# Kernel optimization log

Measured on AMD Instinct MI355X. Metric: run time of the kernel, lower is better.

Reference implementation:

```python
import jax, jax.numpy as jnp
import numpy as np

N = 100000          # nodes
E = 1000000         # edges (before self loops)
F_IN = 128          # node feature dim
HEADS = [4, 2, 2]   # gat_heads
D = 48              # per-head out channels (hardcoded in module)
G = 64              # number of graphs in batch
FC_DIM = 192
OUT_DIM = 96
NEG_SLOPE = 0.2     # PyG GATConv default


def setup_inputs() -> dict:
    key = jax.random.key(0)
    ks = jax.random.split(key, 32)
    d = {
        "x": jax.random.normal(ks[0], (N, F_IN), jnp.float32),
        "edge_index": jax.random.randint(ks[1], (2, E), 0, N, dtype=jnp.int64),
        "batch": jnp.sort(jax.random.randint(ks[2], (N,), 0, G, dtype=jnp.int64)),
    }
    in_ch = F_IN
    k = 3
    for i, h in enumerate(HEADS):
        d[f"W{i}"] = jax.random.normal(ks[k], (in_ch, h * D), jnp.float32) / np.sqrt(in_ch); k += 1
        d[f"att_src{i}"] = jax.random.normal(ks[k], (h, D), jnp.float32) * 0.1; k += 1
        d[f"att_dst{i}"] = jax.random.normal(ks[k], (h, D), jnp.float32) * 0.1; k += 1
        d[f"bias{i}"] = jnp.zeros((h * D,), jnp.float32)
        in_ch = h * D
    d["fcW1"] = jax.random.normal(ks[k], (in_ch, FC_DIM), jnp.float32) / np.sqrt(in_ch); k += 1
    d["fcb1"] = jnp.zeros((FC_DIM,), jnp.float32)
    d["fcW2"] = jax.random.normal(ks[k], (FC_DIM, OUT_DIM), jnp.float32) / np.sqrt(FC_DIM); k += 1
    d["fcb2"] = jnp.zeros((OUT_DIM,), jnp.float32)
    return d


def _gat_layer(x, W, att_src, att_dst, bias, src, dst, heads):
    n = x.shape[0]
    h = (x @ W).reshape(n, heads, D)                    # [N,H,D]
    a_src = jnp.sum(h * att_src, axis=-1)               # [N,H]
    a_dst = jnp.sum(h * att_dst, axis=-1)               # [N,H]
    e = jax.nn.leaky_relu(a_src[src] + a_dst[dst], NEG_SLOPE)   # [Et,H]
    # segment softmax over incoming edges at each destination node
    m = jax.ops.segment_max(e, dst, num_segments=n)
    e = jnp.exp(e - m[dst])
    denom = jax.ops.segment_sum(e, dst, num_segments=n)
    alpha = e / (denom[dst] + 1e-16)                    # [Et,H]
    msg = h[src] * alpha[..., None]                     # [Et,H,D]
    out = jax.ops.segment_sum(msg, dst, num_segments=n) # [N,H,D]
    return out.reshape(n, heads * D) + bias


def reference(x, edge_index, batch,
              W0, att_src0, att_dst0, bias0,
              W1, att_src1, att_dst1, bias1,
              W2, att_src2, att_dst2, bias2,
              fcW1, fcb1, fcW2, fcb2):
    n = x.shape[0]
    loops = jnp.arange(n, dtype=edge_index.dtype)
    src = jnp.concatenate([edge_index[0], loops])   # add self loops (PyG default)
    dst = jnp.concatenate([edge_index[1], loops])
    x = jax.nn.relu(_gat_layer(x, W0, att_src0, att_dst0, bias0, src, dst, HEADS[0]))
    x = jax.nn.relu(_gat_layer(x, W1, att_src1, att_dst1, bias1, src, dst, HEADS[1]))
    x = jax.nn.relu(_gat_layer(x, W2, att_src2, att_dst2, bias2, src, dst, HEADS[2]))
    # global mean pool over graphs
    sums = jax.ops.segment_sum(x, batch, num_segments=G)
    counts = jax.ops.segment_sum(jnp.ones((n, 1), x.dtype), batch, num_segments=G)
    pooled = sums / jnp.maximum(counts, 1.0)
    h = jax.nn.relu(pooled @ fcW1 + fcb1)
    return h @ fcW2 + fcb2
```

## Files before the change

### kernel.cpp

```cpp
#include <hip/hip_runtime.h>

#define CAP 48
#define DD 48
#define BSH 8
#define NBUCK_MAX 400
#define CHUNK_MAX 4300

typedef short v8s __attribute__((ext_vector_type(8)));
typedef float v4f __attribute__((ext_vector_type(4)));
typedef float v2f __attribute__((ext_vector_type(2)));

__device__ __forceinline__ unsigned int bf16r(float f) {
    unsigned int u = __float_as_uint(f);
    return (u + 0x7FFFu + ((u >> 16) & 1u)) >> 16;
}

__device__ __forceinline__ v8s ld_frag(const ushort* p) {
    const uint2* q = reinterpret_cast<const uint2*>(p);
    uint2 a = q[0], b = q[1];
    union { unsigned int u[4]; v8s v; } t;
    t.u[0] = a.x; t.u[1] = a.y; t.u[2] = b.x; t.u[3] = b.y;
    return t.v;
}


__global__ void hist_kernel(const int* __restrict__ ei, int E, int N, int nbuck,
                            int* __restrict__ Hh) {
    __shared__ int lhist[NBUCK_MAX];
    int blk = blockIdx.x, t = threadIdx.x;
    int Et = E + N;
    int chunk = (Et + 255) >> 8;
    int lo = blk * chunk, hi = min(Et, lo + chunk);
    for (int i = t; i < nbuck; i += 256) lhist[i] = 0;
    __syncthreads();
    for (int e = lo + t; e < hi; e += 256) {
        int d = (e < E) ? ei[E + e] : (e - E);
        atomicAdd(&lhist[d >> BSH], 1);
    }
    __syncthreads();
    for (int b = t; b < nbuck; b += 256) Hh[b * 256 + blk] = lhist[b];
}

__global__ void scan_bucket_kernel(int* __restrict__ Hh, int* __restrict__ btot) {
    int b = blockIdx.x, lane = threadIdx.x;
    uint4 v = reinterpret_cast<uint4*>(Hh)[b * 64 + lane];
    unsigned s0 = v.x, s1 = s0 + v.y, s2 = s1 + v.z, s3 = s2 + v.w;
    unsigned incl = s3;
#pragma unroll
    for (int off = 1; off < 64; off <<= 1) {
        unsigned tmp = __shfl_up(incl, off);
        if (lane >= off) incl += tmp;
    }
    unsigned excl = incl - s3;
    reinterpret_cast<uint4*>(Hh)[b * 64 + lane] =
        make_uint4(excl, excl + s0, excl + s1, excl + s2);
    if (lane == 63) btot[b] = (int)incl;
}

__global__ void scan_base_kernel(const int* __restrict__ btot, int* __restrict__ bbase, int nbuck) {
    int lane = threadIdx.x;
    int carry = 0;
    int nch = (nbuck + 63) >> 6;
    for (int c = 0; c < nch; c++) {
        int idx = c * 64 + lane;
        int val = (idx < nbuck) ? btot[idx] : 0;
        int incl = val;
#pragma unroll
        for (int off = 1; off < 64; off <<= 1) {
            int tmp = __shfl_up(incl, off);
            if (lane >= off) incl += tmp;
        }
        if (idx < nbuck) bbase[idx] = carry + incl - val;
        carry += __shfl(incl, 63);
    }
    if (lane == 0) bbase[nbuck] = carry;
}

__global__ void add_base_kernel(int* __restrict__ Hh, const int* __restrict__ bbase) {
    Hh[blockIdx.x * 256 + threadIdx.x] += bbase[blockIdx.x];
}

__global__ void scatter_kernel(const int* __restrict__ ei, int E, int N, int nbuck,
                               const int* __restrict__ Hh, unsigned int* __restrict__ P) {
    __shared__ unsigned int sp[CHUNK_MAX];
    __shared__ int ga[CHUNK_MAX];
    __shared__ int lhist[NBUCK_MAX], lbaseL[NBUCK_MAX], lbaseG[NBUCK_MAX], lcur[NBUCK_MAX];
    int blk = blockIdx.x, t = threadIdx.x;
    int Et = E + N;
    int chunk = (Et + 255) >> 8;
    int lo = blk * chunk, hi = min(Et, lo + chunk);
    for (int i = t; i < nbuck; i += 256) { lhist[i] = 0; lcur[i] = 0; }
    __syncthreads();
    for (int e = lo + t; e < hi; e += 256) {
        int d = (e < E) ? ei[E + e] : (e - E);
        atomicAdd(&lhist[d >> BSH], 1);
    }
    __syncthreads();
    if (t < 64) {
        int lane = t, carry = 0;
        int nch = (nbuck + 63) >> 6;
        for (int c = 0; c < nch; c++) {
            int idx = c * 64 + lane;
            int val = (idx < nbuck) ? lhist[idx] : 0;
            int incl = val;
#pragma unroll
            for (int off = 1; off < 64; off <<= 1) {
                int tmp = __shfl_up(incl, off);
                if (lane >= off) incl += tmp;
            }
            if (idx < nbuck) {
                lbaseL[idx] = carry + incl - val;
                lbaseG[idx] = Hh[idx * 256 + blk];
            }
            carry += __shfl(incl, 63);
        }
    }
    __syncthreads();
    for (int e = lo + t; e < hi; e += 256) {
        int s, d;
        if (e < E) { s = ei[e]; d = ei[E + e]; } else { s = e - E; d = e - E; }
        int b = d >> BSH;
        int lpos = atomicAdd(&lcur[b], 1);
        int loc = lbaseL[b] + lpos;
        sp[loc] = ((unsigned)(d & 255) << 24) | (unsigned)s;
        ga[loc] = lbaseG[b] + lpos;
    }
    __syncthreads();
    int len = hi - lo;
    for (int i = t; i < len; i += 256) P[ga[i]] = sp[i];
}

__global__ void buildadj_kernel(const unsigned int* __restrict__ P, const int* __restrict__ bbase,
                                int* __restrict__ adj, int* __restrict__ cnt, int N) {
    __shared__ int slab[256 * CAP];
    __shared__ int cntL[256];
    int b = blockIdx.x, t = threadIdx.x;
    int n0 = b << BSH;
    int nodes = min(256, N - n0);
    cntL[t] = 0;
    __syncthreads();
    int lo = bbase[b], hi = bbase[b + 1];
    for (int i = lo + t; i < hi; i += 256) {
        unsigned p = P[i];
        int dloc = (int)(p >> 24);
        int s = (int)(p & 0x1FFFFu);
        int lpos = atomicAdd(&cntL[dloc], 1);
        if (lpos < CAP) slab[dloc * CAP + lpos] = s;
    }
    __syncthreads();
    int tot = nodes * CAP;
    for (int i = t; i < tot; i += 256) adj[(long)n0 * CAP + i] = slab[i];
    if (t < nodes) cnt[n0 + t] = min(cntL[t], CAP);
}

__global__ void cast_x_kernel(const float* __restrict__ x, unsigned int* __restrict__ xb, long n2) {
    long i = (long)blockIdx.x * blockDim.x + threadIdx.x;
    if (i >= n2) return;
    float2 v = reinterpret_cast<const float2*>(x)[i];
    xb[i] = bf16r(v.x) | (bf16r(v.y) << 16);
}

__global__ void convw_kernel(const float* __restrict__ W, ushort* __restrict__ WT, int K, int NC) {
    int i = blockIdx.x * blockDim.x + threadIdx.x;
    if (i >= K * NC) return;
    int k = i / NC, n = i % NC;
    WT[n * K + k] = (ushort)bf16r(W[i]);
}

template<int K, int NCT, int HEADS>
__global__ void gemm_mfma(const ushort* __restrict__ Xb, const ushort* __restrict__ WT,
                          const float* __restrict__ att_s, const float* __restrict__ att_d,
                          ushort* __restrict__ Hb, float* __restrict__ asrc,
                          float* __restrict__ adst, int N) {
    __shared__ ushort XT_l[128 * 40];
    __shared__ ushort WT_l[96 * 40];
    int tid = threadIdx.x;
    int wv = tid >> 6, lane = tid & 63;
    int m = lane & 15, quad = lane >> 4;
    int rb = blockIdx.x * 128;
    int c0 = blockIdx.y * 96;
    int mw = wv * 32;
    v4f acc[2][6];
#pragma unroll
    for (int mi = 0; mi < 2; mi++)
#pragma unroll
        for (int nb = 0; nb < 6; nb++) acc[mi][nb] = (v4f){0.f, 0.f, 0.f, 0.f};

    for (int k0 = 0; k0 < K; k0 += 32) {
#pragma unroll
        for (int t = 0; t < 2; t++) {
            int ch = tid + t * 256;
            int r = ch >> 2, kq = ch & 3;
            int rg = rb + r;
            uint4 v = make_uint4(0u, 0u, 0u, 0u);
            if (rg < N) v = *reinterpret_cast<const uint4*>(&Xb[(long)rg * K + k0 + kq * 8]);
            uint2* d = reinterpret_cast<uint2*>(&XT_l[r * 40 + kq * 8]);
            d[0] = make_uint2(v.x, v.y);
            d[1] = make_uint2(v.z, v.w);
        }
#pragma unroll
        for (int t = 0; t < 2; t++) {
            int ch = tid + t * 256;
            if (ch < 384) {
                int wr = ch >> 2, kq = ch & 3;
                uint4 v = *reinterpret_cast<const uint4*>(&WT[(long)(c0 + wr) * K + k0 + kq * 8]);
                uint2* d = reinterpret_cast<uint2*>(&WT_l[wr * 40 + kq * 8]);
                d[0] = make_uint2(v.x, v.y);
                d[1] = make_uint2(v.z, v.w);
            }
        }
        __syncthreads();
        v8s af[2], bf[6];
        af[0] = ld_frag(&XT_l[(mw + m) * 40 + quad * 8]);
        af[1] = ld_frag(&XT_l[(mw + 16 + m) * 40 + quad * 8]);
#pragma unroll
        for (int nb = 0; nb < 6; nb++)
            bf[nb] = ld_frag(&WT_l[(nb * 16 + m) * 40 + quad * 8]);
#pragma unroll
        for (int mi = 0; mi < 2; mi++)
#pragma unroll
            for (int nb = 0; nb < 6; nb++)
                acc[mi][nb] = __builtin_amdgcn_mfma_f32_16x16x32_bf16(af[mi], bf[nb], acc[mi][nb], 0, 0, 0);
        __syncthreads();
    }

#pragma unroll
    for (int mi = 0; mi < 2; mi++)
#pragma unroll
        for (int r = 0; r < 4; r++) {
            int R = rb + mw + mi * 16 + quad * 4 + r;
            if (R < N) {
#pragma unroll
                for (int nb = 0; nb < 6; nb++)
                    Hb[(long)R * NCT + c0 + nb * 16 + m] = (ushort)bf16r(acc[mi][nb][r]);
            }
        }

    float aS[6], aD[6];
    int h0 = c0 / DD;
#pragma unroll
    for (int nb = 0; nb < 6; nb++) {
        int cb = nb * 16 + m;
        int hl = cb / DD;
        int cih = cb - hl * DD;
        aS[nb] = att_s[(h0 + hl) * DD + cih];
        aD[nb] = att_d[(h0 + hl) * DD + cih];
    }
#pragma unroll
    for (int mi = 0; mi < 2; mi++)
#pragma unroll
        for (int r = 0; r < 4; r++) {
            float ps0 = 0.f, ps1 = 0.f, pd0 = 0.f, pd1 = 0.f;
#pragma unroll
            for (int nb = 0; nb < 3; nb++) {
                ps0 = fmaf(acc[mi][nb][r], aS[nb], ps0);
                pd0 = fmaf(acc[mi][nb][r], aD[nb], pd0);
            }
#pragma unroll
            for (int nb = 3; nb < 6; nb++) {
                ps1 = fmaf(acc[mi][nb][r], aS[nb], ps1);
                pd1 = fmaf(acc[mi][nb][r], aD[nb], pd1);
            }
#pragma unroll
            for (int d = 1; d < 16; d <<= 1) {
                ps0 += __shfl_xor(ps0, d); ps1 += __shfl_xor(ps1, d);
                pd0 += __shfl_xor(pd0, d); pd1 += __shfl_xor(pd1, d);
            }
            int R = rb + mw + mi * 16 + quad * 4 + r;
            if (m == 0 && R < N) {
                asrc[R * HEADS + h0]     = ps0;
                asrc[R * HEADS + h0 + 1] = ps1;
                adst[R * HEADS + h0]     = pd0;
                adst[R * HEADS + h0 + 1] = pd1;
            }
        }
}

template<int OUT, int HEADS, int EPW, bool OBF16>
__global__ void agg_kernel(const unsigned int* __restrict__ Hb,
                           const float* __restrict__ asrc, const float* __restrict__ adst,
                           const int* __restrict__ adj, const int* __restrict__ cnt,
                           const float* __restrict__ bias,
                           unsigned int* __restrict__ Ob, float* __restrict__ Of, int N) {
    constexpr int LPE = 64 / EPW;
    constexpr int ROWU = OUT / 2;
    static_assert(LPE * 6 == ROWU, "lane chunk is 6 uints");
    __shared__ float wlds[4][HEADS][65];
    __shared__ int   slds[4][64];
    int wv = threadIdx.x >> 6;
    int lane = threadIdx.x & 63;
    int esub = lane / LPE;
    int lp   = lane % LPE;
    int n = blockIdx.x * 4 + wv;
    bool valid = (n < N);
    int nn = valid ? n : 0;
    int deg_raw = cnt[nn];
    int araw = (lane < CAP) ? adj[(long)nn * CAP + lane] : 0;
    int deg = min(deg_raw, CAP);
    int s = (lane < deg) ? araw : 0;
    slds[wv][lane] = s;
    __builtin_amdgcn_wave_barrier();

    int c = lp * 12;
    int head = c / DD;

    uint3 A0, A1, B0, B1;
    {
        int s0 = slds[wv][esub];
        int s1 = slds[wv][EPW + esub];
        const unsigned int* p0 = &Hb[(long)s0 * ROWU + lp * 6];
        const unsigned int* p1 = &Hb[(long)s1 * ROWU + lp * 6];
        A0 = *reinterpret_cast<const uint3*>(p0);
        A1 = *reinterpret_cast<const uint3*>(p0 + 3);
        B0 = *reinterpret_cast<const uint3*>(p1);
        B1 = *reinterpret_cast<const uint3*>(p1 + 3);
    }

    float av[HEADS], dvv[HEADS];
    if constexpr (HEADS == 4) {
        float4 t = *reinterpret_cast<const float4*>(&asrc[s * 4]);
        av[0] = t.x; av[1] = t.y; av[2] = t.z; av[3] = t.w;
        float4 u = *reinterpret_cast<const float4*>(&adst[nn * 4]);
        dvv[0] = u.x; dvv[1] = u.y; dvv[2] = u.z; dvv[3] = u.w;
    } else {
        float2 t = *reinterpret_cast<const float2*>(&asrc[s * 2]);
        av[0] = t.x; av[1] = t.y;
        float2 u = *reinterpret_cast<const float2*>(&adst[nn * 2]);
        dvv[0] = u.x; dvv[1] = u.y;
    }
    float w[HEADS], den[HEADS];
#pragma unroll
    for (int h = 0; h < HEADS; h++) {
        float e = av[h] + dvv[h];
        e = (e < 0.f) ? 0.2f * e : e;
        w[h] = (lane < deg) ? __expf(e) : 0.f;
        wlds[wv][h][lane] = w[h];
    }
#pragma unroll
    for (int h = 0; h < HEADS; h++) {
        float dsum = w[h];
#pragma unroll
        for (int off = 1; off < 64; off <<= 1) dsum += __shfl_xor(dsum, off);
        den[h] = dsum;
    }
    __builtin_amdgcn_wave_barrier();

    const float* wrow = &wlds[wv][head][0];
    v2f a0 = (v2f){0.f, 0.f}, a1 = (v2f){0.f, 0.f}, a2 = (v2f){0.f, 0.f};
    v2f a3 = (v2f){0.f, 0.f}, a4 = (v2f){0.f, 0.f}, a5 = (v2f){0.f, 0.f};

    auto ACC6 = [&](const uint3& lo, const uint3& hi, float wgt) {
        v2f p;
        p.x = __uint_as_float(lo.x << 16); p.y = __uint_as_float(lo.x & 0xFFFF0000u); a0 += wgt * p;
        p.x = __uint_as_float(lo.y << 16); p.y = __uint_as_float(lo.y & 0xFFFF0000u); a1 += wgt * p;
        p.x = __uint_as_float(lo.z << 16); p.y = __uint_as_float(lo.z & 0xFFFF0000u); a2 += wgt * p;
        p.x = __uint_as_float(hi.x << 16); p.y = __uint_as_float(hi.x & 0xFFFF0000u); a3 += wgt * p;
        p.x = __uint_as_float(hi.y << 16); p.y = __uint_as_float(hi.y & 0xFFFF0000u); a4 += wgt * p;
        p.x = __uint_as_float(hi.z << 16); p.y = __uint_as_float(hi.z & 0xFFFF0000u); a5 += wgt * p;
    };

    int nb = (deg + 2 * EPW - 1) / (2 * EPW);
    for (int it = 0; it < nb; it++) {
        int nbase = (it + 1) * 2 * EPW;
        uint3 nA0, nA1, nB0, nB1;
        {
            int s0n = slds[wv][nbase + esub];
            int s1n = slds[wv][nbase + EPW + esub];
            const unsigned int* p0 = &Hb[(long)s0n * ROWU + lp * 6];
            const unsigned int* p1 = &Hb[(long)s1n * ROWU + lp * 6];
            nA0 = *reinterpret_cast<const uint3*>(p0);
            nA1 = *reinterpret_cast<const uint3*>(p0 + 3);
            nB0 = *reinterpret_cast<const uint3*>(p1);
            nB1 = *reinterpret_cast<const uint3*>(p1 + 3);
        }
        int e0 = it * 2 * EPW + esub;
        float w0 = wrow[e0], w1 = wrow[e0 + EPW];
        ACC6(A0, A1, w0);
        ACC6(B0, B1, w1);
        A0 = nA0; A1 = nA1; B0 = nB0; B1 = nB1;
    }

#pragma unroll
    for (int off = LPE; off < 64; off <<= 1) {
        a0.x += __shfl_xor(a0.x, off); a0.y += __shfl_xor(a0.y, off);
        a1.x += __shfl_xor(a1.x, off); a1.y += __shfl_xor(a1.y, off);
        a2.x += __shfl_xor(a2.x, off); a2.y += __shfl_xor(a2.y, off);
        a3.x += __shfl_xor(a3.x, off); a3.y += __shfl_xor(a3.y, off);
        a4.x += __shfl_xor(a4.x, off); a4.y += __shfl_xor(a4.y, off);
        a5.x += __shfl_xor(a5.x, off); a5.y += __shfl_xor(a5.y, off);
    }

    if (valid && esub == 0) {
        float denh;
        if constexpr (HEADS == 4) {
            denh = (head == 0) ? den[0] : (head == 1) ? den[1] : (head == 2) ? den[2] : den[3];
        } else {
            denh = (head == 0) ? den[0] : den[1];
        }
        float invd = 1.f / (denh + 1e-16f);
        float o[12];
        o[0]  = fmaxf(fmaf(a0.x, invd, bias[c + 0]), 0.f);
        o[1]  = fmaxf(fmaf(a0.y, invd, bias[c + 1]), 0.f);
        o[2]  = fmaxf(fmaf(a1.x, invd, bias[c + 2]), 0.f);
        o[3]  = fmaxf(fmaf(a1.y, invd, bias[c + 3]), 0.f);
        o[4]  = fmaxf(fmaf(a2.x, invd, bias[c + 4]), 0.f);
        o[5]  = fmaxf(fmaf(a2.y, invd, bias[c + 5]), 0.f);
        o[6]  = fmaxf(fmaf(a3.x, invd, bias[c + 6]), 0.f);
        o[7]  = fmaxf(fmaf(a3.y, invd, bias[c + 7]), 0.f);
        o[8]  = fmaxf(fmaf(a4.x, invd, bias[c + 8]), 0.f);
        o[9]  = fmaxf(fmaf(a4.y, invd, bias[c + 9]), 0.f);
        o[10] = fmaxf(fmaf(a5.x, invd, bias[c + 10]), 0.f);
        o[11] = fmaxf(fmaf(a5.y, invd, bias[c + 11]), 0.f);
        if (OBF16) {
            uint3 pk1, pk2;
            pk1.x = bf16r(o[0])  | (bf16r(o[1])  << 16);
            pk1.y = bf16r(o[2])  | (bf16r(o[3])  << 16);
            pk1.z = bf16r(o[4])  | (bf16r(o[5])  << 16);
            pk2.x = bf16r(o[6])  | (bf16r(o[7])  << 16);
            pk2.y = bf16r(o[8])  | (bf16r(o[9])  << 16);
            pk2.z = bf16r(o[10]) | (bf16r(o[11]) << 16);
            unsigned int* dst = &Ob[(long)n * ROWU + lp * 6];
            *reinterpret_cast<uint3*>(dst)     = pk1;
            *reinterpret_cast<uint3*>(dst + 3) = pk2;
        } else {
            float* dst = &Of[(long)n * OUT + c];
            *reinterpret_cast<float4*>(dst)     = make_float4(o[0], o[1], o[2],  o[3]);
            *reinterpret_cast<float4*>(dst + 4) = make_float4(o[4], o[5], o[6],  o[7]);
            *reinterpret_cast<float4*>(dst + 8) = make_float4(o[8], o[9], o[10], o[11]);
        }
    }
}

__global__ void pool_kernel(const float* __restrict__ O, const int* __restrict__ batch,
                            float* __restrict__ sums, float* __restrict__ counts, int N) {
    int grp = threadIdx.x >> 7;
    int c = threadIdx.x & 127;
    int n0 = (blockIdx.x * 4 + grp) * 64;
    if (n0 >= N) return;
    int nend = min(N, n0 + 64);
    bool act = (c < 96);
    float acc = 0.f; int cl = 0;
    int cur = batch[n0];
    int n = n0;
    for (; n + 4 <= nend; n += 4) {
        int g0 = batch[n], g1 = batch[n + 1], g2 = batch[n + 2], g3 = batch[n + 3];
        float v0 = 0.f, v1 = 0.f, v2 = 0.f, v3 = 0.f;
        if (act) {
            v0 = O[(long)n * 96 + c];       v1 = O[(long)(n + 1) * 96 + c];
            v2 = O[(long)(n + 2) * 96 + c]; v3 = O[(long)(n + 3) * 96 + c];
        }
#define POOL_STEP(g, v)                                                        \
        if ((g) != cur) {                                                      \
            if (act) atomicAdd(&sums[cur * 96 + c], acc);                      \
            if (c == 96) atomicAdd(&counts[cur], (float)cl);                   \
            acc = 0.f; cl = 0; cur = (g);                                      \
        }                                                                      \
        acc += (v); cl++;
        POOL_STEP(g0, v0) POOL_STEP(g1, v1) POOL_STEP(g2, v2) POOL_STEP(g3, v3)
    }
    for (; n < nend; n++) {
        int g = batch[n];
        float v = act ? O[(long)n * 96 + c] : 0.f;
        POOL_STEP(g, v)
    }
#undef POOL_STEP
    if (act) atomicAdd(&sums[cur * 96 + c], acc);
    if (c == 96) atomicAdd(&counts[cur], (float)cl);
}

__global__ void fc_kernel(const float* __restrict__ sums, const float* __restrict__ counts,
                          const float* __restrict__ W1, const float* __restrict__ b1,
                          const float* __restrict__ W2, const float* __restrict__ b2,
                          float* __restrict__ out) {
    __shared__ float p[96];
    __shared__ float h1[192];
    int g = blockIdx.x, tid = threadIdx.x;
    if (tid < 96) p[tid] = sums[g * 96 + tid] / fmaxf(counts[g], 1.0f);
    __syncthreads();
    float s = b1[tid];
    for (int c = 0; c < 96; c++) s = fmaf(p[c], W1[c * 192 + tid], s);
    h1[tid] = fmaxf(s, 0.f);
    __syncthreads();
    if (tid < 96) {
        float s2 = b2[tid];
        for (int j = 0; j < 192; j++) s2 = fmaf(h1[j], W2[j * 96 + tid], s2);
        out[g * 96 + tid] = s2;
    }
}

extern "C" void kernel_launch(void* const* d_in, const int* in_sizes, int n_in,
                              void* d_out, int out_size, void* d_ws, size_t ws_size,
                              hipStream_t stream) {
    const float* x     = (const float*)d_in[0];
    const int*   ei    = (const int*)d_in[1];
    const int*   batch = (const int*)d_in[2];
    const float* W0  = (const float*)d_in[3];
    const float* as0 = (const float*)d_in[4];
    const float* ad0 = (const float*)d_in[5];
    const float* b0  = (const float*)d_in[6];
    const float* W1  = (const float*)d_in[7];
    const float* as1 = (const float*)d_in[8];
    const float* ad1 = (const float*)d_in[9];
    const float* b1  = (const float*)d_in[10];
    const float* W2  = (const float*)d_in[11];
    const float* as2 = (const float*)d_in[12];
    const float* ad2 = (const float*)d_in[13];
    const float* b2  = (const float*)d_in[14];
    const float* fcW1 = (const float*)d_in[15];
    const float* fcb1 = (const float*)d_in[16];
    const float* fcW2 = (const float*)d_in[17];
    const float* fcb2 = (const float*)d_in[18];

    const int N = in_sizes[0] / 128;
    const int E = in_sizes[1] / 2;
    const int Et = E + N;
    const int nbuck = (N + 255) >> 8;

    char* ws = (char*)d_ws;
    unsigned int* Xb   = (unsigned int*)ws;
    unsigned int* Hb   = (unsigned int*)(ws + (size_t)N * 256);
    unsigned int* Ob   = (unsigned int*)(ws + (size_t)N * 640);
    float*        Obuf = (float*)(ws + (size_t)N * 1024);
    float*        ASRC = (float*)(ws + (size_t)N * 1408);
    float*        ADST = (float*)(ws + (size_t)N * 1424);
    int*          ADJ  = (int*)(ws + (size_t)N * 1440);
    int*          CNT  = (int*)(ws + (size_t)N * 1632);
    float*        SUMS = (float*)(ws + (size_t)N * 1636);
    float*        COUNTS = SUMS + 64 * 96;
    ushort*       WT0  = (ushort*)(COUNTS + 64);
    ushort*       WT1  = WT0 + 192 * 128;
    ushort*       WT2  = WT1 + 96 * 192;
    char*         tail = (char*)(WT2 + 96 * 96);
    int*          HIST = (int*)tail;
    int*          BTOT = (int*)(tail + NBUCK_MAX * 256 * 4);
    int*          BBASE = (int*)(tail + NBUCK_MAX * 256 * 4 + NBUCK_MAX * 4);
    unsigned int* P    = (unsigned int*)(tail + NBUCK_MAX * 260 * 4 + 64);

    hipMemsetAsync(SUMS, 0, (64 * 96 + 64) * 4, stream);

    hist_kernel<<<256, 256, 0, stream>>>(ei, E, N, nbuck, HIST);
    scan_bucket_kernel<<<nbuck, 64, 0, stream>>>(HIST, BTOT);
    scan_base_kernel<<<1, 64, 0, stream>>>(BTOT, BBASE, nbuck);
    add_base_kernel<<<nbuck, 256, 0, stream>>>(HIST, BBASE);
    scatter_kernel<<<256, 256, 0, stream>>>(ei, E, N, nbuck, HIST, P);
    buildadj_kernel<<<nbuck, 256, 0, stream>>>(P, BBASE, ADJ, CNT, N);

    long n2 = (long)N * 64;
    cast_x_kernel<<<(int)((n2 + 255) / 256), 256, 0, stream>>>(x, Xb, n2);
    convw_kernel<<<(128 * 192 + 255) / 256, 256, 0, stream>>>(W0, WT0, 128, 192);
    convw_kernel<<<(192 * 96 + 255) / 256, 256, 0, stream>>>(W1, WT1, 192, 96);
    convw_kernel<<<(96 * 96 + 255) / 256, 256, 0, stream>>>(W2, WT2, 96, 96);

    int gb = (N + 127) / 128;

    gemm_mfma<128, 192, 4><<<dim3(gb, 2), 256, 0, stream>>>((const ushort*)Xb, WT0, as0, ad0,
                                                            (ushort*)Hb, ASRC, ADST, N);
    agg_kernel<192, 4, 4, true><<<(N + 3) / 4, 256, 0, stream>>>(Hb, ASRC, ADST, ADJ, CNT, b0, Ob, nullptr, N);

    gemm_mfma<192, 96, 2><<<dim3(gb, 1), 256, 0, stream>>>((const ushort*)Ob, WT1, as1, ad1,
                                                           (ushort*)Hb, ASRC, ADST, N);
    agg_kernel<96, 2, 8, true><<<(N + 3) / 4, 256, 0, stream>>>(Hb, ASRC, ADST, ADJ, CNT, b1, Ob, nullptr, N);

    gemm_mfma<96, 96, 2><<<dim3(gb, 1), 256, 0, stream>>>((const ushort*)Ob, WT2, as2, ad2,
                                                          (ushort*)Hb, ASRC, ADST, N);
    agg_kernel<96, 2, 8, false><<<(N + 3) / 4, 256, 0, stream>>>(Hb, ASRC, ADST, ADJ, CNT, b2, nullptr, Obuf, N);

    pool_kernel<<<(N / 256) + 1, 512, 0, stream>>>(Obuf, batch, SUMS, COUNTS, N);
    fc_kernel<<<64, 192, 0, stream>>>(SUMS, COUNTS, fcW1, fcb1, fcW2, fcb2, (float*)d_out);
}
```

Baseline: 472.7 us.

## Compact adjacency to CSR, fold attention into GEMM, bf16 final layer output

Adjacency storage changes from a fixed 48-slot padded slab per node to a compact CSR layout with packed start and degree, and the aggregation skips neighbor row loads past the degree. The attention projections are folded into W as four extra GEMM columns (computed by a new attw kernel), which drops the shuffle-reduction epilogue. The final aggregation now writes bf16 instead of fp32, and the pooling kernel reads packed bf16. The GEMM grid is flattened with interleaved column blocks. These changes cut memory traffic and epilogue work, at the cost of bf16 rounding in the attention logits and the pooled features, plus one extra MFMA column tile.

Result: no change. 474.6 us (+0.4%).

```diff
diff --git a/kernel.cpp b/kernel.cpp
--- a/kernel.cpp
+++ b/kernel.cpp
@@ -131,9 +131,10 @@
 }
 
 __global__ void buildadj_kernel(const unsigned int* __restrict__ P, const int* __restrict__ bbase,
-                                int* __restrict__ adj, int* __restrict__ cnt, int N) {
+                                int* __restrict__ adj, int* __restrict__ cro, int N) {
     __shared__ int slab[256 * CAP];
     __shared__ int cntL[256];
+    __shared__ int wsum[4];
     int b = blockIdx.x, t = threadIdx.x;
     int n0 = b << BSH;
     int nodes = min(256, N - n0);
@@ -148,9 +149,26 @@
         if (lpos < CAP) slab[dloc * CAP + lpos] = s;
     }
     __syncthreads();
-    int tot = nodes * CAP;
-    for (int i = t; i < tot; i += 256) adj[(long)n0 * CAP + i] = slab[i];
-    if (t < nodes) cnt[n0 + t] = min(cntL[t], CAP);
+    int capped = min(cntL[t], CAP);
+    int lane = t & 63, wv = t >> 6;
+    int incl = capped;
+#pragma unroll
+    for (int off = 1; off < 64; off <<= 1) {
+        int tmp = __shfl_up(incl, off);
+        if (lane >= off) incl += tmp;
+    }
+    if (lane == 63) wsum[wv] = incl;
+    __syncthreads();
+    int wbase = 0;
+    if (wv > 0) wbase += wsum[0];
+    if (wv > 1) wbase += wsum[1];
+    if (wv > 2) wbase += wsum[2];
+    int startL = wbase + incl - capped;
+    if (t < nodes) {
+        int start = n0 * CAP + startL;
+        cro[n0 + t] = start | (capped << 25);
+        for (int j = 0; j < capped; j++) adj[start + j] = slab[t * CAP + j];
+    }
 }
 
 __global__ void cast_x_kernel(const float* __restrict__ x, unsigned int* __restrict__ xb, long n2) {
@@ -167,24 +185,40 @@
     WT[n * K + k] = (ushort)bf16r(W[i]);
 }
 
-template<int K, int NCT, int HEADS>
+__global__ void attw_kernel(const float* __restrict__ W, const float* __restrict__ as_,
+                            const float* __restrict__ ad_, ushort* __restrict__ WT,
+                            int K, int NC, int H2) {
+    int tid = blockIdx.x * blockDim.x + threadIdx.x;
+    if (tid >= K * H2) return;
+    int k = tid / H2, idx = tid % H2;
+    int h = idx >> 1;
+    const float* att = (idx & 1) ? ad_ : as_;
+    float s = 0.f;
+    for (int d = 0; d < 48; d++) s += W[k * NC + h * 48 + d] * att[h * 48 + d];
+    WT[(long)(NC + idx) * K + k] = (ushort)bf16r(s);
+}
+
+template<int K, int NCT, int HEADS, int NBY>
 __global__ void gemm_mfma(const ushort* __restrict__ Xb, const ushort* __restrict__ WT,
-                          const float* __restrict__ att_s, const float* __restrict__ att_d,
                           ushort* __restrict__ Hb, float* __restrict__ asrc,
                           float* __restrict__ adst, int N) {
     __shared__ ushort XT_l[128 * 40];
-    __shared__ ushort WT_l[96 * 40];
+    __shared__ ushort WT_l[112 * 40];
     int tid = threadIdx.x;
     int wv = tid >> 6, lane = tid & 63;
     int m = lane & 15, quad = lane >> 4;
-    int rb = blockIdx.x * 128;
-    int c0 = blockIdx.y * 96;
+    int bid = blockIdx.x;
+    int ybl = (NBY == 2) ? (bid & 1) : 0;
+    int xbl = (NBY == 2) ? (bid >> 1) : bid;
+    int rb = xbl * 128;
+    int c0 = ybl * 96;
+    int h0 = 2 * ybl;
     int mw = wv * 32;
-    v4f acc[2][6];
+    v4f acc[2][7];
 #pragma unroll
     for (int mi = 0; mi < 2; mi++)
 #pragma unroll
-        for (int nb = 0; nb < 6; nb++) acc[mi][nb] = (v4f){0.f, 0.f, 0.f, 0.f};
+        for (int nb = 0; nb < 7; nb++) acc[mi][nb] = (v4f){0.f, 0.f, 0.f, 0.f};
 
     for (int k0 = 0; k0 < K; k0 += 32) {
 #pragma unroll
@@ -201,25 +235,29 @@
 #pragma unroll
         for (int t = 0; t < 2; t++) {
             int ch = tid + t * 256;
-            if (ch < 384) {
+            if (ch < 448) {
                 int wr = ch >> 2, kq = ch & 3;
-                uint4 v = *reinterpret_cast<const uint4*>(&WT[(long)(c0 + wr) * K + k0 + kq * 8]);
+                uint4 v = make_uint4(0u, 0u, 0u, 0u);
+                if (wr < 96)
+                    v = *reinterpret_cast<const uint4*>(&WT[(long)(c0 + wr) * K + k0 + kq * 8]);
+                else if (wr < 100)
+                    v = *reinterpret_cast<const uint4*>(&WT[(long)(NCT + 4 * ybl + (wr - 96)) * K + k0 + kq * 8]);
                 uint2* d = reinterpret_cast<uint2*>(&WT_l[wr * 40 + kq * 8]);
                 d[0] = make_uint2(v.x, v.y);
                 d[1] = make_uint2(v.z, v.w);
             }
         }
         __syncthreads();
-        v8s af[2], bf[6];
+        v8s af[2], bf[7];
         af[0] = ld_frag(&XT_l[(mw + m) * 40 + quad * 8]);
         af[1] = ld_frag(&XT_l[(mw + 16 + m) * 40 + quad * 8]);
 #pragma unroll
-        for (int nb = 0; nb < 6; nb++)
+        for (int nb = 0; nb < 7; nb++)
             bf[nb] = ld_frag(&WT_l[(nb * 16 + m) * 40 + quad * 8]);
 #pragma unroll
         for (int mi = 0; mi < 2; mi++)
 #pragma unroll
-            for (int nb = 0; nb < 6; nb++)
+            for (int nb = 0; nb < 7; nb++)
                 acc[mi][nb] = __builtin_amdgcn_mfma_f32_16x16x32_bf16(af[mi], bf[nb], acc[mi][nb], 0, 0, 0);
         __syncthreads();
     }
@@ -236,42 +274,16 @@
             }
         }
 
-    float aS[6], aD[6];
-    int h0 = c0 / DD;
-#pragma unroll
-    for (int nb = 0; nb < 6; nb++) {
-        int cb = nb * 16 + m;
-        int hl = cb / DD;
-        int cih = cb - hl * DD;
-        aS[nb] = att_s[(h0 + hl) * DD + cih];
-        aD[nb] = att_d[(h0 + hl) * DD + cih];
-    }
 #pragma unroll
     for (int mi = 0; mi < 2; mi++)
 #pragma unroll
         for (int r = 0; r < 4; r++) {
-            float ps0 = 0.f, ps1 = 0.f, pd0 = 0.f, pd1 = 0.f;
-#pragma unroll
-            for (int nb = 0; nb < 3; nb++) {
-                ps0 = fmaf(acc[mi][nb][r], aS[nb], ps0);
-                pd0 = fmaf(acc[mi][nb][r], aD[nb], pd0);
-            }
-#pragma unroll
-            for (int nb = 3; nb < 6; nb++) {
-                ps1 = fmaf(acc[mi][nb][r], aS[nb], ps1);
-                pd1 = fmaf(acc[mi][nb][r], aD[nb], pd1);
-            }
-#pragma unroll
-            for (int d = 1; d < 16; d <<= 1) {
-                ps0 += __shfl_xor(ps0, d); ps1 += __shfl_xor(ps1, d);
-                pd0 += __shfl_xor(pd0, d); pd1 += __shfl_xor(pd1, d);
-            }
             int R = rb + mw + mi * 16 + quad * 4 + r;
-            if (m == 0 && R < N) {
-                asrc[R * HEADS + h0]     = ps0;
-                asrc[R * HEADS + h0 + 1] = ps1;
-                adst[R * HEADS + h0]     = pd0;
-                adst[R * HEADS + h0 + 1] = pd1;
+            if (m < 4 && R < N) {
+                float v = acc[mi][6][r];
+                int h = h0 + (m >> 1);
+                if (m & 1) adst[R * HEADS + h] = v;
+                else       asrc[R * HEADS + h] = v;
             }
         }
 }
@@ -279,7 +291,7 @@
 template<int OUT, int HEADS, int EPW, bool OBF16>
 __global__ void agg_kernel(const unsigned int* __restrict__ Hb,
                            const float* __restrict__ asrc, const float* __restrict__ adst,
-                           const int* __restrict__ adj, const int* __restrict__ cnt,
+                           const int* __restrict__ adj, const int* __restrict__ cro,
                            const float* __restrict__ bias,
                            unsigned int* __restrict__ Ob, float* __restrict__ Of, int N) {
     constexpr int LPE = 64 / EPW;
@@ -294,10 +306,11 @@
     int n = blockIdx.x * 4 + wv;
     bool valid = (n < N);
     int nn = valid ? n : 0;
-    int deg_raw = cnt[nn];
-    int araw = (lane < CAP) ? adj[(long)nn * CAP + lane] : 0;
-    int deg = min(deg_raw, CAP);
-    int s = (lane < deg) ? araw : 0;
+    unsigned craw = (unsigned)cro[nn];
+    int deg = (int)(craw >> 25);
+    int start = (int)(craw & 0x1FFFFFFu);
+    int s = 0;
+    if (lane < deg) s = adj[start + lane];
     slds[wv][lane] = s;
     __builtin_amdgcn_wave_barrier();
 
@@ -305,15 +318,18 @@
     int head = c / DD;
 
     uint3 A0, A1, B0, B1;
+    B0 = make_uint3(0u, 0u, 0u); B1 = B0;
     {
         int s0 = slds[wv][esub];
-        int s1 = slds[wv][EPW + esub];
         const unsigned int* p0 = &Hb[(long)s0 * ROWU + lp * 6];
-        const unsigned int* p1 = &Hb[(long)s1 * ROWU + lp * 6];
         A0 = *reinterpret_cast<const uint3*>(p0);
         A1 = *reinterpret_cast<const uint3*>(p0 + 3);
-        B0 = *reinterpret_cast<const uint3*>(p1);
-        B1 = *reinterpret_cast<const uint3*>(p1 + 3);
+        if (EPW < deg) {
+            int s1 = slds[wv][EPW + esub];
+            const unsigned int* p1 = &Hb[(long)s1 * ROWU + lp * 6];
+            B0 = *reinterpret_cast<const uint3*>(p1);
+            B1 = *reinterpret_cast<const uint3*>(p1 + 3);
+        }
     }
 
     float av[HEADS], dvv[HEADS];
@@ -362,16 +378,18 @@
     int nb = (deg + 2 * EPW - 1) / (2 * EPW);
     for (int it = 0; it < nb; it++) {
         int nbase = (it + 1) * 2 * EPW;
-        uint3 nA0, nA1, nB0, nB1;
-        {
+        uint3 nA0 = make_uint3(0u, 0u, 0u), nA1 = nA0, nB0 = nA0, nB1 = nA0;
+        if (nbase < deg) {
             int s0n = slds[wv][nbase + esub];
-            int s1n = slds[wv][nbase + EPW + esub];
             const unsigned int* p0 = &Hb[(long)s0n * ROWU + lp * 6];
-            const unsigned int* p1 = &Hb[(long)s1n * ROWU + lp * 6];
             nA0 = *reinterpret_cast<const uint3*>(p0);
             nA1 = *reinterpret_cast<const uint3*>(p0 + 3);
-            nB0 = *reinterpret_cast<const uint3*>(p1);
-            nB1 = *reinterpret_cast<const uint3*>(p1 + 3);
+            if (nbase + EPW < deg) {
+                int s1n = slds[wv][nbase + EPW + esub];
+                const unsigned int* p1 = &Hb[(long)s1n * ROWU + lp * 6];
+                nB0 = *reinterpret_cast<const uint3*>(p1);
+                nB1 = *reinterpret_cast<const uint3*>(p1 + 3);
+            }
         }
         int e0 = it * 2 * EPW + esub;
         float w0 = wrow[e0], w1 = wrow[e0 + EPW];
@@ -431,41 +449,36 @@
     }
 }
 
-__global__ void pool_kernel(const float* __restrict__ O, const int* __restrict__ batch,
+__global__ void pool_kernel(const unsigned int* __restrict__ Ob, const int* __restrict__ batch,
                             float* __restrict__ sums, float* __restrict__ counts, int N) {
-    int grp = threadIdx.x >> 7;
-    int c = threadIdx.x & 127;
-    int n0 = (blockIdx.x * 4 + grp) * 64;
+    int grp = threadIdx.x >> 6;
+    int lane = threadIdx.x & 63;
+    int n0 = (blockIdx.x * 8 + grp) * 64;
     if (n0 >= N) return;
     int nend = min(N, n0 + 64);
-    bool act = (c < 96);
-    float acc = 0.f; int cl = 0;
+    bool act = (lane < 48);
+    float ax = 0.f, ay = 0.f; int cl = 0;
     int cur = batch[n0];
-    int n = n0;
-    for (; n + 4 <= nend; n += 4) {
-        int g0 = batch[n], g1 = batch[n + 1], g2 = batch[n + 2], g3 = batch[n + 3];
-        float v0 = 0.f, v1 = 0.f, v2 = 0.f, v3 = 0.f;
-        if (act) {
-            v0 = O[(long)n * 96 + c];       v1 = O[(long)(n + 1) * 96 + c];
-            v2 = O[(long)(n + 2) * 96 + c]; v3 = O[(long)(n + 3) * 96 + c];
-        }
-#define POOL_STEP(g, v)                                                        \
-        if ((g) != cur) {                                                      \
-            if (act) atomicAdd(&sums[cur * 96 + c], acc);                      \
-            if (c == 96) atomicAdd(&counts[cur], (float)cl);                   \
-            acc = 0.f; cl = 0; cur = (g);                                      \
-        }                                                                      \
-        acc += (v); cl++;
-        POOL_STEP(g0, v0) POOL_STEP(g1, v1) POOL_STEP(g2, v2) POOL_STEP(g3, v3)
-    }
-    for (; n < nend; n++) {
+    for (int n = n0; n < nend; n++) {
         int g = batch[n];
-        float v = act ? O[(long)n * 96 + c] : 0.f;
-        POOL_STEP(g, v)
-    }
-#undef POOL_STEP
-    if (act) atomicAdd(&sums[cur * 96 + c], acc);
-    if (c == 96) atomicAdd(&counts[cur], (float)cl);
+        unsigned v = act ? Ob[(long)n * 48 + lane] : 0u;
+        float vx = __uint_as_float(v << 16);
+        float vy = __uint_as_float(v & 0xFFFF0000u);
+        if (g != cur) {
+            if (act) {
+                atomicAdd(&sums[cur * 96 + lane * 2],     ax);
+                atomicAdd(&sums[cur * 96 + lane * 2 + 1], ay);
+            }
+            if (lane == 48) atomicAdd(&counts[cur], (float)cl);
+            ax = 0.f; ay = 0.f; cl = 0; cur = g;
+        }
+        ax += vx; ay += vy; cl++;
+    }
+    if (act) {
+        atomicAdd(&sums[cur * 96 + lane * 2],     ax);
+        atomicAdd(&sums[cur * 96 + lane * 2 + 1], ay);
+    }
+    if (lane == 48) atomicAdd(&counts[cur], (float)cl);
 }
 
 __global__ void fc_kernel(const float* __restrict__ sums, const float* __restrict__ counts,
@@ -513,24 +526,22 @@
 
     const int N = in_sizes[0] / 128;
     const int E = in_sizes[1] / 2;
-    const int Et = E + N;
     const int nbuck = (N + 255) >> 8;
 
     char* ws = (char*)d_ws;
     unsigned int* Xb   = (unsigned int*)ws;
     unsigned int* Hb   = (unsigned int*)(ws + (size_t)N * 256);
     unsigned int* Ob   = (unsigned int*)(ws + (size_t)N * 640);
-    float*        Obuf = (float*)(ws + (size_t)N * 1024);
     float*        ASRC = (float*)(ws + (size_t)N * 1408);
     float*        ADST = (float*)(ws + (size_t)N * 1424);
     int*          ADJ  = (int*)(ws + (size_t)N * 1440);
-    int*          CNT  = (int*)(ws + (size_t)N * 1632);
+    int*          CRO  = (int*)(ws + (size_t)N * 1632);
     float*        SUMS = (float*)(ws + (size_t)N * 1636);
     float*        COUNTS = SUMS + 64 * 96;
     ushort*       WT0  = (ushort*)(COUNTS + 64);
-    ushort*       WT1  = WT0 + 192 * 128;
-    ushort*       WT2  = WT1 + 96 * 192;
-    char*         tail = (char*)(WT2 + 96 * 96);
+    ushort*       WT1  = WT0 + 200 * 128;
+    ushort*       WT2  = WT1 + 100 * 192;
+    char*         tail = (char*)(WT2 + 100 * 96);
     int*          HIST = (int*)tail;
     int*          BTOT = (int*)(tail + NBUCK_MAX * 256 * 4);
     int*          BBASE = (int*)(tail + NBUCK_MAX * 256 * 4 + NBUCK_MAX * 4);
@@ -543,28 +554,31 @@
     scan_base_kernel<<<1, 64, 0, stream>>>(BTOT, BBASE, nbuck);
     add_base_kernel<<<nbuck, 256, 0, stream>>>(HIST, BBASE);
     scatter_kernel<<<256, 256, 0, stream>>>(ei, E, N, nbuck, HIST, P);
-    buildadj_kernel<<<nbuck, 256, 0, stream>>>(P, BBASE, ADJ, CNT, N);
+    buildadj_kernel<<<nbuck, 256, 0, stream>>>(P, BBASE, ADJ, CRO, N);
 
     long n2 = (long)N * 64;
     cast_x_kernel<<<(int)((n2 + 255) / 256), 256, 0, stream>>>(x, Xb, n2);
     convw_kernel<<<(128 * 192 + 255) / 256, 256, 0, stream>>>(W0, WT0, 128, 192);
     convw_kernel<<<(192 * 96 + 255) / 256, 256, 0, stream>>>(W1, WT1, 192, 96);
     convw_kernel<<<(96 * 96 + 255) / 256, 256, 0, stream>>>(W2, WT2, 96, 96);
+    attw_kernel<<<4, 256, 0, stream>>>(W0, as0, ad0, WT0, 128, 192, 8);
+    attw_kernel<<<3, 256, 0, stream>>>(W1, as1, ad1, WT1, 192, 96, 4);
+    attw_kernel<<<2, 256, 0, stream>>>(W2, as2, ad2, WT2, 96, 96, 4);
 
     int gb = (N + 127) / 128;
 
-    gemm_mfma<128, 192, 4><<<dim3(gb, 2), 256, 0, stream>>>((const ushort*)Xb, WT0, as0, ad0,
-                                                            (ushort*)Hb, ASRC, ADST, N);
-    agg_kernel<192, 4, 4, true><<<(N + 3) / 4, 256, 0, stream>>>(Hb, ASRC, ADST, ADJ, CNT, b0, Ob, nullptr, N);
-
-    gemm_mfma<192, 96, 2><<<dim3(gb, 1), 256, 0, stream>>>((const ushort*)Ob, WT1, as1, ad1,
-                                                           (ushort*)Hb, ASRC, ADST, N);
-    agg_kernel<96, 2, 8, true><<<(N + 3) / 4, 256, 0, stream>>>(Hb, ASRC, ADST, ADJ, CNT, b1, Ob, nullptr, N);
-
-    gemm_mfma<96, 96, 2><<<dim3(gb, 1), 256, 0, stream>>>((const ushort*)Ob, WT2, as2, ad2,
+    gemm_mfma<128, 192, 4, 2><<<gb * 2, 256, 0, stream>>>((const ushort*)Xb, WT0,
                                                           (ushort*)Hb, ASRC, ADST, N);
-    agg_kernel<96, 2, 8, false><<<(N + 3) / 4, 256, 0, stream>>>(Hb, ASRC, ADST, ADJ, CNT, b2, nullptr, Obuf, N);
-
-    pool_kernel<<<(N / 256) + 1, 512, 0, stream>>>(Obuf, batch, SUMS, COUNTS, N);
+    agg_kernel<192, 4, 4, true><<<(N + 3) / 4, 256, 0, stream>>>(Hb, ASRC, ADST, ADJ, CRO, b0, Ob, nullptr, N);
+
+    gemm_mfma<192, 96, 2, 1><<<gb, 256, 0, stream>>>((const ushort*)Ob, WT1,
+                                                     (ushort*)Hb, ASRC, ADST, N);
+    agg_kernel<96, 2, 8, true><<<(N + 3) / 4, 256, 0, stream>>>(Hb, ASRC, ADST, ADJ, CRO, b1, Ob, nullptr, N);
+
+    gemm_mfma<96, 96, 2, 1><<<gb, 256, 0, stream>>>((const ushort*)Ob, WT2,
+                                                    (ushort*)Hb, ASRC, ADST, N);
+    agg_kernel<96, 2, 8, true><<<(N + 3) / 4, 256, 0, stream>>>(Hb, ASRC, ADST, ADJ, CRO, b2, Ob, nullptr, N);
+
+    pool_kernel<<<(N + 511) / 512, 512, 0, stream>>>(Ob, batch, SUMS, COUNTS, N);
     fc_kernel<<<64, 192, 0, stream>>>(SUMS, COUNTS, fcW1, fcb1, fcW2, fcb2, (float*)d_out);
 }
```
